# Kernel optimization log

Hardware: AMD Instinct MI355X
Metric: run time of the kernel (lower is better)

The kernel has to match this reference:

```python
import jax, jax.numpy as jnp
import numpy as np

# Grid derived from defaults: pc_range=(0,-40,-3,70.4,40,1), voxel=(0.2,0.2,4)
GX, GY = 352, 400          # round((70.4-0)/0.2), round((40-(-40))/0.2)
B, P = 4, 65536            # samples, points per sample
NSEG = B * GX * GY + 1     # dense pillar-id space + 1 sentinel for masked points
OUT_CH = 64
BN_EPS = 1e-3


def setup_inputs() -> dict:
    key = jax.random.key(0)
    k1, k2, k3 = jax.random.split(key, 3)
    xyz_min = jnp.array([0.0, -40.0, -3.0], jnp.float32)
    xyz_max = jnp.array([70.4, 40.0, 1.0], jnp.float32)
    xyz = jax.random.uniform(k1, (B, P, 3), jnp.float32, minval=xyz_min, maxval=xyz_max)
    rest = jax.random.normal(k2, (B, P, 4), jnp.float32)  # rcs, v_r, v_r_comp, time
    points = jnp.concatenate([xyz, rest], axis=-1)        # [B, P, 7]
    W = jax.random.normal(k3, (OUT_CH, 13), jnp.float32) * (1.0 / np.sqrt(13.0))
    gamma = jnp.ones((OUT_CH,), jnp.float32)
    beta = jnp.zeros((OUT_CH,), jnp.float32)
    return {"points": points, "W": W, "gamma": gamma, "beta": beta}


def reference(points, W, gamma, beta):
    Bn, Pn, _ = points.shape
    pts = points.reshape(Bn * Pn, 7)                      # [N, 7] (= torch points[:, 1:])
    dtype = pts.dtype
    voxel = jnp.array([0.2, 0.2, 4.0], dtype)
    pc_min = jnp.array([0.0, -40.0, -3.0], dtype)
    batch_idx = jnp.repeat(jnp.arange(Bn, dtype=jnp.int32), Pn)

    coords_f = (pts[:, :3] - pc_min) / voxel              # float voxel coords
    mask = ((coords_f[:, 0] >= 0) & (coords_f[:, 0] < GX)
            & (coords_f[:, 1] >= 0) & (coords_f[:, 1] < GY))
    coords = coords_f.astype(jnp.int32)                   # [N, 3] (cx, cy, cz)
    sentinel = Bn * GX * GY                               # trash segment for masked points
    lin = jnp.where(mask,
                    batch_idx * (GX * GY) + coords[:, 0] * GY + coords[:, 1],
                    sentinel)
    # torch.unique(..., return_inverse=True, dim=0) on (batch, cx, cy) rows ==
    # unique of the bijective linear id (same sorted order).
    unq, unq_inv = jnp.unique(lin, return_inverse=True, size=NSEG, fill_value=sentinel)

    cnt = jax.ops.segment_sum(jnp.ones((lin.shape[0], 1), dtype), unq_inv, num_segments=NSEG)
    mean_xyz = jax.ops.segment_sum(pts[:, :3], unq_inv, num_segments=NSEG) / jnp.maximum(cnt, 1.0)
    f_cluster = pts[:, :3] - mean_xyz[unq_inv]
    f_center = pts[:, :3] - (coords.astype(dtype) * voxel + voxel * 0.5 + pc_min)
    feats = jnp.concatenate([pts, f_cluster, f_center], axis=-1)   # [N, 13]

    # PFN layer (last_layer=True): Linear -> BN1d (training stats) -> ReLU
    x = feats @ W.T                                       # [N, 64]
    mu = x.mean(axis=0)
    var = x.var(axis=0)                                   # biased, as BN training
    x = jax.nn.relu((x - mu) * jax.lax.rsqrt(var + BN_EPS) * gamma + beta)

    fmax = jax.ops.segment_max(x, unq_inv, num_segments=NSEG)     # scatter_max
    x_max = fmax[unq_inv]                                 # gather back (PFN output)
    feat_max = jax.ops.segment_max(x_max, unq_inv, num_segments=NSEG)

    valid = (unq < sentinel)[:, None]                     # real pillars only
    feat_max = jnp.where(valid, feat_max, 0.0)            # padded/empty -> 0

    b = unq // (GX * GY)
    rem = unq % (GX * GY)
    cx = rem // GY
    cy = rem % GY
    coords_out = jnp.stack([b, cy, cx], axis=1).astype(jnp.int32)  # (batch, y, x)
    grid_size = jnp.array([GY, GX], jnp.int32)
    return feat_max, coords_out, grid_size
```

## Files before the change

kernel.cpp:

```cpp
#include <hip/hip_runtime.h>
#include <stdint.h>
#include <utility>

#define NPTS   262144
#define GXGY   140800
#define GYv    400
#define NSEG   563201
#define SENT   563200
#define NB_SCAN 275
#define PIL_BLOCKS 2048
#define MOM_BLOCKS 512

constexpr size_t alignup(size_t x) { return (x + 255) & ~(size_t)255; }
constexpr size_t O_CNT  = 0;
constexpr size_t O_SUMS = alignup(O_CNT + (size_t)NSEG * 4);
constexpr size_t O_MOM  = alignup(O_SUMS + (size_t)NSEG * 12);
constexpr size_t ZERO_BYTES = alignup(O_MOM + 104 * 4);
constexpr size_t O_PPTR = ZERO_BYTES;
constexpr size_t O_LINA = alignup(O_PPTR + (size_t)NSEG * 4);
constexpr size_t O_ROWI = alignup(O_LINA + (size_t)NPTS * 4);
constexpr size_t O_FEAT = alignup(O_ROWI + (size_t)NPTS * 16);
constexpr size_t O_BSO  = alignup(O_FEAT + (size_t)NPTS * 64);
constexpr size_t O_BSC  = alignup(O_BSO + NB_SCAN * 4);
constexpr size_t O_KP   = alignup(O_BSC + NB_SCAN * 4);
constexpr size_t O_WF   = alignup(O_KP + 256);
constexpr size_t O_SH   = alignup(O_WF + 832 * 4);

__device__ __forceinline__ int point_lin(float x, float y, int b, bool& mask) {
  float cxf = x / 0.2f;
  float cyf = (y + 40.0f) / 0.2f;
  int cx = (int)cxf, cy = (int)cyf;
  mask = (cxf >= 0.0f) && (cxf < 352.0f) && (cyf >= 0.0f) && (cyf < 400.0f);
  return mask ? (b * GXGY + cx * GYv + cy) : SENT;
}

__global__ __launch_bounds__(256) void k_count(const float* __restrict__ pts,
                                               unsigned int* __restrict__ cnt,
                                               float* __restrict__ sums,
                                               unsigned int* __restrict__ lina) {
  int i = blockIdx.x * 256 + threadIdx.x;
  if (i >= NPTS) return;
  const float* p = pts + (size_t)i * 7;
  float x = p[0], y = p[1], z = p[2];
  bool m;
  int lin = point_lin(x, y, i >> 16, m);
  lina[i] = (unsigned)lin;
  atomicAdd(&cnt[lin], 1u);
  atomicAdd(&sums[lin * 3 + 0], x);
  atomicAdd(&sums[lin * 3 + 1], y);
  atomicAdd(&sums[lin * 3 + 2], z);
}

__global__ __launch_bounds__(256) void k_scan1(const unsigned int* __restrict__ cnt,
                                               unsigned int* __restrict__ bso,
                                               unsigned int* __restrict__ bsc) {
  int t = threadIdx.x;
  int base = blockIdx.x * 2048 + t * 8;
  const uint4* c4 = (const uint4*)(cnt + base);
  uint4 a = c4[0], b = c4[1];
  unsigned so = (a.x > 0) + (a.y > 0) + (a.z > 0) + (a.w > 0) +
                (b.x > 0) + (b.y > 0) + (b.z > 0) + (b.w > 0);
  unsigned sc = a.x + a.y + a.z + a.w + b.x + b.y + b.z + b.w;
  for (int m = 1; m < 64; m <<= 1) { so += __shfl_xor(so, m); sc += __shfl_xor(sc, m); }
  __shared__ unsigned wo[4], wc[4];
  if ((t & 63) == 0) { wo[t >> 6] = so; wc[t >> 6] = sc; }
  __syncthreads();
  if (t == 0) {
    bso[blockIdx.x] = wo[0] + wo[1] + wo[2] + wo[3];
    bsc[blockIdx.x] = wc[0] + wc[1] + wc[2] + wc[3];
  }
}

__global__ __launch_bounds__(256) void k_scan3(const unsigned int* __restrict__ cnt,
                                               const unsigned int* __restrict__ bso,
                                               const unsigned int* __restrict__ bsc,
                                               uint4* __restrict__ rowinfo,
                                               unsigned int* __restrict__ pptr,
                                               unsigned int* __restrict__ kp) {
  int t = threadIdx.x;
  unsigned vo_m = 0, vc_m = 0, vo_a = 0;
  for (int e = t; e < NB_SCAN; e += 256) {
    unsigned o = bso[e], c = bsc[e];
    vo_a += o;
    if (e < (int)blockIdx.x) { vo_m += o; vc_m += c; }
  }
  for (int m = 1; m < 64; m <<= 1) {
    vo_m += __shfl_xor(vo_m, m);
    vc_m += __shfl_xor(vc_m, m);
    vo_a += __shfl_xor(vo_a, m);
  }
  __shared__ unsigned s0[4], s1[4], s2[4];
  int wv = t >> 6;
  if ((t & 63) == 0) { s0[wv] = vo_m; s1[wv] = vc_m; s2[wv] = vo_a; }
  __syncthreads();
  unsigned boo = s0[0] + s0[1] + s0[2] + s0[3];
  unsigned boc = s1[0] + s1[1] + s1[2] + s1[3];
  unsigned tot = s2[0] + s2[1] + s2[2] + s2[3];
  if (blockIdx.x == 0 && t == 0) *kp = tot;

  int base = blockIdx.x * 2048 + t * 8;
  const uint4* q = (const uint4*)(cnt + base);
  uint4 a = q[0], b = q[1];
  unsigned c[8] = {a.x, a.y, a.z, a.w, b.x, b.y, b.z, b.w};
  unsigned po[8], pc[8];
  unsigned so = 0, sc = 0;
#pragma unroll
  for (int k = 0; k < 8; k++) {
    po[k] = so; pc[k] = sc;
    so += (c[k] > 0); sc += c[k];
  }
  __shared__ unsigned sdo[256], sdc[256];
  __syncthreads();
  sdo[t] = so; sdc[t] = sc;
  __syncthreads();
  for (int off = 1; off < 256; off <<= 1) {
    unsigned ao = (t >= off) ? sdo[t - off] : 0u;
    unsigned ac = (t >= off) ? sdc[t - off] : 0u;
    __syncthreads();
    sdo[t] += ao; sdc[t] += ac;
    __syncthreads();
  }
  unsigned eo = sdo[t] - so + boo;
  unsigned ec = sdc[t] - sc + boc;
#pragma unroll
  for (int k = 0; k < 8; k++) {
    if (c[k] > 0) {
      unsigned r = eo + po[k];
      unsigned start = ec + pc[k];
      rowinfo[r] = make_uint4((unsigned)(base + k), start, c[k], 0u);
      pptr[base + k] = start;
    }
  }
}

__global__ __launch_bounds__(256) void k_sortfeat(const float* __restrict__ pts,
                                                  const unsigned int* __restrict__ lina,
                                                  const unsigned int* __restrict__ cnt,
                                                  const float* __restrict__ sums,
                                                  unsigned int* __restrict__ pptr,
                                                  float* __restrict__ feat) {
  int i = blockIdx.x * 256 + threadIdx.x;
  if (i >= NPTS) return;
  unsigned lin = lina[i];
  if (lin == SENT) return;
  const float* p = pts + (size_t)i * 7;
  float x = p[0], y = p[1], z = p[2];
  unsigned pos = atomicAdd(&pptr[lin], 1u);
  float cm = fmaxf((float)cnt[lin], 1.0f);
  float m0 = sums[lin * 3 + 0] / cm;
  float m1 = sums[lin * 3 + 1] / cm;
  float m2 = sums[lin * 3 + 2] / cm;
  int cx = (int)(x / 0.2f);
  int cy = (int)((y + 40.0f) / 0.2f);
  int cz = (int)((z + 3.0f) / 4.0f);
  float4 A = make_float4(x, y, z, p[3]);
  float4 B = make_float4(p[4], p[5], p[6], x - m0);
  float4 C = make_float4(y - m1, z - m2,
                         x - ((float)cx * 0.2f + 0.1f + 0.0f),
                         y - ((float)cy * 0.2f + 0.1f - 40.0f));
  float4 D = make_float4(z - ((float)cz * 4.0f + 2.0f - 3.0f), 0.f, 0.f, 0.f);
  float4* fb = (float4*)(feat + (size_t)pos * 16);
  fb[0] = A; fb[1] = B; fb[2] = C; fb[3] = D;
}

constexpr int tri_j(int t) { int j = 0; while (t >= 13 - j) { t -= 13 - j; j++; } return j; }
constexpr int tri_k(int t) { int j = 0; while (t >= 13 - j) { t -= 13 - j; j++; } return j + t; }

template<int G, size_t U>
__device__ __forceinline__ void accum_one(const float (&f)[13], float (&acc)[52]) {
  constexpr int E = G * 52 + (int)U;
  if constexpr (E < 13) {
    acc[U] += f[E];
  } else {
    constexpr int J = tri_j(E - 13);
    constexpr int K = tri_k(E - 13);
    acc[U] += f[J] * f[K];
  }
}
template<int G, size_t... Us>
__device__ __forceinline__ void accum_all(const float (&f)[13], float (&acc)[52],
                                          std::index_sequence<Us...>) {
  (accum_one<G, Us>(f, acc), ...);
}

template<int G>
__device__ __forceinline__ void moments_body(const float* __restrict__ feat,
                                             float* __restrict__ mom, int chunk) {
  float acc[52];
#pragma unroll
  for (int u = 0; u < 52; u++) acc[u] = 0.f;
#pragma unroll
  for (int r = 0; r < 4; r++) {
    int i = chunk * 1024 + r * 256 + threadIdx.x;
    const float4* fp = (const float4*)(feat + (size_t)i * 16);
    float4 A = fp[0], B = fp[1], C = fp[2], D = fp[3];
    float f[13] = {A.x, A.y, A.z, A.w, B.x, B.y, B.z, B.w, C.x, C.y, C.z, C.w, D.x};
    accum_all<G>(f, acc, std::make_index_sequence<52>{});
  }
  __shared__ float red[4][52];
  int wv = threadIdx.x >> 6, lane = threadIdx.x & 63;
#pragma unroll
  for (int u = 0; u < 52; u++) {
    float v = acc[u];
    v += __shfl_xor(v, 1);  v += __shfl_xor(v, 2);  v += __shfl_xor(v, 4);
    v += __shfl_xor(v, 8);  v += __shfl_xor(v, 16); v += __shfl_xor(v, 32);
    if (lane == 0) red[wv][u] = v;
  }
  __syncthreads();
  if (threadIdx.x < 52) {
    int u = threadIdx.x;
    atomicAdd(&mom[G * 52 + u], red[0][u] + red[1][u] + red[2][u] + red[3][u]);
  }
}

__global__ __launch_bounds__(256, 2) void k_moments(const float* __restrict__ feat,
                                                    float* __restrict__ mom) {
  int chunk = blockIdx.x >> 1;
  if ((blockIdx.x & 1) == 0) moments_body<0>(feat, mom, chunk);
  else                       moments_body<1>(feat, mom, chunk);
}

__global__ void k_bnfinal(const float* __restrict__ W,
                          const float* __restrict__ g,
                          const float* __restrict__ bta,
                          const float* __restrict__ mom,
                          float* __restrict__ wf,
                          float* __restrict__ sh) {
  int c = threadIdx.x;
  float w[13];
#pragma unroll
  for (int j = 0; j < 13; j++) w[j] = W[c * 13 + j];
  const float invN = 1.0f / (float)NPTS;
  float mu = 0.f;
#pragma unroll
  for (int j = 0; j < 13; j++) mu += w[j] * (mom[j] * invN);
  float e2 = 0.f;
  int mi = 13;
#pragma unroll
  for (int j = 0; j < 13; j++) {
#pragma unroll
    for (int k = j; k < 13; k++) {
      float coef = (j == k) ? 1.0f : 2.0f;
      e2 += coef * w[j] * w[k] * mom[mi];
      mi++;
    }
  }
  e2 *= invN;
  float var = e2 - mu * mu;
  float rsig = 1.0f / sqrtf(var + 1e-3f);
  float sc = g[c] * rsig;
#pragma unroll
  for (int j = 0; j < 13; j++) wf[c * 13 + j] = w[j] * sc;
  sh[c] = bta[c] - mu * sc;
}

__global__ __launch_bounds__(256) void k_pillar(const float* __restrict__ wf,
                                                const float* __restrict__ sh,
                                                const uint4* __restrict__ rowinfo,
                                                const unsigned int* __restrict__ kp_p,
                                                const float* __restrict__ feat,
                                                float* __restrict__ out) {
  int tid = threadIdx.x;
  int lane = tid & 15;
  int ch0 = lane * 4;
  float wr[52];
  float shv[4];
#pragma unroll
  for (int c4 = 0; c4 < 4; c4++) {
    shv[c4] = sh[ch0 + c4];
#pragma unroll
    for (int j = 0; j < 13; j++) wr[c4 * 13 + j] = wf[(ch0 + c4) * 13 + j];
  }
  unsigned kp = *kp_p;

  const int NGRP = PIL_BLOCKS * 16;
  for (int r = blockIdx.x * 16 + (tid >> 4); r < NSEG; r += NGRP) {
    float m0 = -3.4e38f, m1 = -3.4e38f, m2 = -3.4e38f, m3 = -3.4e38f;
    int b = 4, cy = 0, cx = 0;
    if ((unsigned)r < kp) {
      uint4 ri = rowinfo[r];
      unsigned id = ri.x, start = ri.y, n = ri.z;
      b = id / GXGY;
      unsigned rem = id - (unsigned)b * GXGY;
      cx = rem / GYv;
      cy = rem - cx * GYv;
      const float4* fb = (const float4*)(feat + (size_t)start * 16);
      for (unsigned p = 0; p < n; p++) {
        float4 A = fb[0], B = fb[1], C = fb[2], D = fb[3];
        fb += 4;
        float d0, d1, d2, d3;
#define DOT(dst, c4)                                                          \
        dst = shv[c4];                                                        \
        dst += wr[c4 * 13 + 0]  * A.x;  dst += wr[c4 * 13 + 1]  * A.y;        \
        dst += wr[c4 * 13 + 2]  * A.z;  dst += wr[c4 * 13 + 3]  * A.w;        \
        dst += wr[c4 * 13 + 4]  * B.x;  dst += wr[c4 * 13 + 5]  * B.y;        \
        dst += wr[c4 * 13 + 6]  * B.z;  dst += wr[c4 * 13 + 7]  * B.w;        \
        dst += wr[c4 * 13 + 8]  * C.x;  dst += wr[c4 * 13 + 9]  * C.y;        \
        dst += wr[c4 * 13 + 10] * C.z;  dst += wr[c4 * 13 + 11] * C.w;        \
        dst += wr[c4 * 13 + 12] * D.x;
        DOT(d0, 0) DOT(d1, 1) DOT(d2, 2) DOT(d3, 3)
#undef DOT
        m0 = fmaxf(m0, d0); m1 = fmaxf(m1, d1);
        m2 = fmaxf(m2, d2); m3 = fmaxf(m3, d3);
      }
    }
    float4 v = make_float4(fmaxf(m0, 0.f), fmaxf(m1, 0.f),
                           fmaxf(m2, 0.f), fmaxf(m3, 0.f));
    *(float4*)(out + (size_t)r * 64 + lane * 4) = v;
    if (lane == 0) {
      float* cc = out + (size_t)NSEG * 64 + (size_t)r * 3;
      cc[0] = (float)b;
      cc[1] = (float)cy;
      cc[2] = (float)cx;
    }
  }
  if (blockIdx.x == 0 && tid == 0) {
    float* g = out + (size_t)NSEG * 67;
    g[0] = 400.0f;
    g[1] = 352.0f;
  }
}

extern "C" void kernel_launch(void* const* d_in, const int* in_sizes, int n_in,
                              void* d_out, int out_size, void* d_ws, size_t ws_size,
                              hipStream_t stream) {
  const float* pts = (const float*)d_in[0];
  const float* W   = (const float*)d_in[1];
  const float* g   = (const float*)d_in[2];
  const float* bta = (const float*)d_in[3];
  float* out = (float*)d_out;
  char* ws = (char*)d_ws;

  unsigned int* cnt  = (unsigned int*)(ws + O_CNT);
  float*        sums = (float*)(ws + O_SUMS);
  float*        mom  = (float*)(ws + O_MOM);
  unsigned int* pptr = (unsigned int*)(ws + O_PPTR);
  unsigned int* lina = (unsigned int*)(ws + O_LINA);
  uint4*        rowi = (uint4*)(ws + O_ROWI);
  float*        feat = (float*)(ws + O_FEAT);
  unsigned int* bso  = (unsigned int*)(ws + O_BSO);
  unsigned int* bsc  = (unsigned int*)(ws + O_BSC);
  unsigned int* kp   = (unsigned int*)(ws + O_KP);
  float*        wf   = (float*)(ws + O_WF);
  float*        sh   = (float*)(ws + O_SH);
  (void)in_sizes; (void)n_in; (void)out_size; (void)ws_size;

  hipMemsetAsync(ws, 0, ZERO_BYTES, stream);

  k_count   <<<NPTS / 256, 256, 0, stream>>>(pts, cnt, sums, lina);
  k_scan1   <<<NB_SCAN, 256, 0, stream>>>(cnt, bso, bsc);
  k_scan3   <<<NB_SCAN, 256, 0, stream>>>(cnt, bso, bsc, rowi, pptr, kp);
  k_sortfeat<<<NPTS / 256, 256, 0, stream>>>(pts, lina, cnt, sums, pptr, feat);
  k_moments <<<MOM_BLOCKS, 256, 0, stream>>>(feat, mom);
  k_bnfinal <<<1, 64, 0, stream>>>(W, g, bta, mom, wf, sh);
  k_pillar  <<<PIL_BLOCKS, 256, 0, stream>>>(wf, sh, rowi, kp, feat, out);
}
```

Baseline: 287.9 us.

## Fuse moments into sort-feature kernel and fold BN finalize into pillar kernel

Feature-moment accumulation now happens while features are built in the scatter kernel, so the separate pass that re-reads the whole feature buffer goes away. The batch-norm finalize kernel is removed: every pillar block recomputes scale and shift from the moments and raw weights in shared memory, then applies scale and shift after the dot product. Two launches are removed, but 1024 blocks now issue atomics to the moments buffer, every pillar block redoes the finalize, and each point's max step gains an extra multiply-add. Masked points now also contribute to the moments, matching the earlier behaviour where sentinel slots were counted.

```diff
diff --git a/kernel.cpp b/kernel.cpp
--- a/kernel.cpp
+++ b/kernel.cpp
@@ -9,7 +9,6 @@
 #define SENT   563200
 #define NB_SCAN 275
 #define PIL_BLOCKS 2048
-#define MOM_BLOCKS 512
 
 constexpr size_t alignup(size_t x) { return (x + 255) & ~(size_t)255; }
 constexpr size_t O_CNT  = 0;
@@ -23,8 +22,6 @@
 constexpr size_t O_BSO  = alignup(O_FEAT + (size_t)NPTS * 64);
 constexpr size_t O_BSC  = alignup(O_BSO + NB_SCAN * 4);
 constexpr size_t O_KP   = alignup(O_BSC + NB_SCAN * 4);
-constexpr size_t O_WF   = alignup(O_KP + 256);
-constexpr size_t O_SH   = alignup(O_WF + 832 * 4);
 
 __device__ __forceinline__ int point_lin(float x, float y, int b, bool& mask) {
   float cxf = x / 0.2f;
@@ -133,19 +130,56 @@
   }
 }
 
-__global__ __launch_bounds__(256) void k_sortfeat(const float* __restrict__ pts,
-                                                  const unsigned int* __restrict__ lina,
-                                                  const unsigned int* __restrict__ cnt,
-                                                  const float* __restrict__ sums,
-                                                  unsigned int* __restrict__ pptr,
-                                                  float* __restrict__ feat) {
+constexpr int tri_j(int t) { int j = 0; while (t >= 13 - j) { t -= 13 - j; j++; } return j; }
+constexpr int tri_k(int t) { int j = 0; while (t >= 13 - j) { t -= 13 - j; j++; } return j + t; }
+
+template<int G, size_t U>
+__device__ __forceinline__ void accum_one(const float (&f)[13], float (&acc)[52]) {
+  constexpr int E = G * 52 + (int)U;
+  if constexpr (E < 13) {
+    acc[U] = f[E];
+  } else {
+    constexpr int J = tri_j(E - 13);
+    constexpr int K = tri_k(E - 13);
+    acc[U] = f[J] * f[K];
+  }
+}
+template<int G, size_t... Us>
+__device__ __forceinline__ void accum_all(const float (&f)[13], float (&acc)[52],
+                                          std::index_sequence<Us...>) {
+  (accum_one<G, Us>(f, acc), ...);
+}
+
+__device__ __forceinline__ void block_reduce_acc(float (&acc)[52],
+                                                 float* __restrict__ mom, int base) {
+  __shared__ float red[4][52];
+  int wv = threadIdx.x >> 6, lane = threadIdx.x & 63;
+#pragma unroll
+  for (int u = 0; u < 52; u++) {
+    float v = acc[u];
+    v += __shfl_xor(v, 1);  v += __shfl_xor(v, 2);  v += __shfl_xor(v, 4);
+    v += __shfl_xor(v, 8);  v += __shfl_xor(v, 16); v += __shfl_xor(v, 32);
+    if (lane == 0) red[wv][u] = v;
+  }
+  __syncthreads();
+  if (threadIdx.x < 52) {
+    int u = threadIdx.x;
+    atomicAdd(&mom[base + u], red[0][u] + red[1][u] + red[2][u] + red[3][u]);
+  }
+  __syncthreads();
+}
+
+__global__ __launch_bounds__(256, 2) void k_sfm(const float* __restrict__ pts,
+                                                const unsigned int* __restrict__ lina,
+                                                const unsigned int* __restrict__ cnt,
+                                                const float* __restrict__ sums,
+                                                unsigned int* __restrict__ pptr,
+                                                float* __restrict__ feat,
+                                                float* __restrict__ mom) {
   int i = blockIdx.x * 256 + threadIdx.x;
-  if (i >= NPTS) return;
   unsigned lin = lina[i];
-  if (lin == SENT) return;
   const float* p = pts + (size_t)i * 7;
   float x = p[0], y = p[1], z = p[2];
-  unsigned pos = atomicAdd(&pptr[lin], 1u);
   float cm = fmaxf((float)cnt[lin], 1.0f);
   float m0 = sums[lin * 3 + 0] / cm;
   float m1 = sums[lin * 3 + 1] / cm;
@@ -153,123 +187,73 @@
   int cx = (int)(x / 0.2f);
   int cy = (int)((y + 40.0f) / 0.2f);
   int cz = (int)((z + 3.0f) / 4.0f);
-  float4 A = make_float4(x, y, z, p[3]);
-  float4 B = make_float4(p[4], p[5], p[6], x - m0);
-  float4 C = make_float4(y - m1, z - m2,
-                         x - ((float)cx * 0.2f + 0.1f + 0.0f),
-                         y - ((float)cy * 0.2f + 0.1f - 40.0f));
-  float4 D = make_float4(z - ((float)cz * 4.0f + 2.0f - 3.0f), 0.f, 0.f, 0.f);
-  float4* fb = (float4*)(feat + (size_t)pos * 16);
-  fb[0] = A; fb[1] = B; fb[2] = C; fb[3] = D;
-}
-
-constexpr int tri_j(int t) { int j = 0; while (t >= 13 - j) { t -= 13 - j; j++; } return j; }
-constexpr int tri_k(int t) { int j = 0; while (t >= 13 - j) { t -= 13 - j; j++; } return j + t; }
-
-template<int G, size_t U>
-__device__ __forceinline__ void accum_one(const float (&f)[13], float (&acc)[52]) {
-  constexpr int E = G * 52 + (int)U;
-  if constexpr (E < 13) {
-    acc[U] += f[E];
-  } else {
-    constexpr int J = tri_j(E - 13);
-    constexpr int K = tri_k(E - 13);
-    acc[U] += f[J] * f[K];
-  }
-}
-template<int G, size_t... Us>
-__device__ __forceinline__ void accum_all(const float (&f)[13], float (&acc)[52],
-                                          std::index_sequence<Us...>) {
-  (accum_one<G, Us>(f, acc), ...);
-}
-
-template<int G>
-__device__ __forceinline__ void moments_body(const float* __restrict__ feat,
-                                             float* __restrict__ mom, int chunk) {
+  float f[13] = {x, y, z, p[3], p[4], p[5], p[6],
+                 x - m0, y - m1, z - m2,
+                 x - ((float)cx * 0.2f + 0.1f + 0.0f),
+                 y - ((float)cy * 0.2f + 0.1f - 40.0f),
+                 z - ((float)cz * 4.0f + 2.0f - 3.0f)};
+  if (lin != SENT) {
+    unsigned pos = atomicAdd(&pptr[lin], 1u);
+    float4* fb = (float4*)(feat + (size_t)pos * 16);
+    fb[0] = make_float4(f[0], f[1], f[2], f[3]);
+    fb[1] = make_float4(f[4], f[5], f[6], f[7]);
+    fb[2] = make_float4(f[8], f[9], f[10], f[11]);
+    fb[3] = make_float4(f[12], 0.f, 0.f, 0.f);
+  }
   float acc[52];
-#pragma unroll
-  for (int u = 0; u < 52; u++) acc[u] = 0.f;
-#pragma unroll
-  for (int r = 0; r < 4; r++) {
-    int i = chunk * 1024 + r * 256 + threadIdx.x;
-    const float4* fp = (const float4*)(feat + (size_t)i * 16);
-    float4 A = fp[0], B = fp[1], C = fp[2], D = fp[3];
-    float f[13] = {A.x, A.y, A.z, A.w, B.x, B.y, B.z, B.w, C.x, C.y, C.z, C.w, D.x};
-    accum_all<G>(f, acc, std::make_index_sequence<52>{});
-  }
-  __shared__ float red[4][52];
-  int wv = threadIdx.x >> 6, lane = threadIdx.x & 63;
-#pragma unroll
-  for (int u = 0; u < 52; u++) {
-    float v = acc[u];
-    v += __shfl_xor(v, 1);  v += __shfl_xor(v, 2);  v += __shfl_xor(v, 4);
-    v += __shfl_xor(v, 8);  v += __shfl_xor(v, 16); v += __shfl_xor(v, 32);
-    if (lane == 0) red[wv][u] = v;
-  }
-  __syncthreads();
-  if (threadIdx.x < 52) {
-    int u = threadIdx.x;
-    atomicAdd(&mom[G * 52 + u], red[0][u] + red[1][u] + red[2][u] + red[3][u]);
-  }
-}
-
-__global__ __launch_bounds__(256, 2) void k_moments(const float* __restrict__ feat,
-                                                    float* __restrict__ mom) {
-  int chunk = blockIdx.x >> 1;
-  if ((blockIdx.x & 1) == 0) moments_body<0>(feat, mom, chunk);
-  else                       moments_body<1>(feat, mom, chunk);
-}
-
-__global__ void k_bnfinal(const float* __restrict__ W,
-                          const float* __restrict__ g,
-                          const float* __restrict__ bta,
-                          const float* __restrict__ mom,
-                          float* __restrict__ wf,
-                          float* __restrict__ sh) {
-  int c = threadIdx.x;
-  float w[13];
-#pragma unroll
-  for (int j = 0; j < 13; j++) w[j] = W[c * 13 + j];
-  const float invN = 1.0f / (float)NPTS;
-  float mu = 0.f;
-#pragma unroll
-  for (int j = 0; j < 13; j++) mu += w[j] * (mom[j] * invN);
-  float e2 = 0.f;
-  int mi = 13;
-#pragma unroll
-  for (int j = 0; j < 13; j++) {
-#pragma unroll
-    for (int k = j; k < 13; k++) {
-      float coef = (j == k) ? 1.0f : 2.0f;
-      e2 += coef * w[j] * w[k] * mom[mi];
-      mi++;
-    }
-  }
-  e2 *= invN;
-  float var = e2 - mu * mu;
-  float rsig = 1.0f / sqrtf(var + 1e-3f);
-  float sc = g[c] * rsig;
-#pragma unroll
-  for (int j = 0; j < 13; j++) wf[c * 13 + j] = w[j] * sc;
-  sh[c] = bta[c] - mu * sc;
-}
-
-__global__ __launch_bounds__(256) void k_pillar(const float* __restrict__ wf,
-                                                const float* __restrict__ sh,
+  accum_all<0>(f, acc, std::make_index_sequence<52>{});
+  block_reduce_acc(acc, mom, 0);
+  accum_all<1>(f, acc, std::make_index_sequence<52>{});
+  block_reduce_acc(acc, mom, 52);
+}
+
+__global__ __launch_bounds__(256) void k_pillar(const float* __restrict__ W,
+                                                const float* __restrict__ g,
+                                                const float* __restrict__ bta,
+                                                const float* __restrict__ mom,
                                                 const uint4* __restrict__ rowinfo,
                                                 const unsigned int* __restrict__ kp_p,
                                                 const float* __restrict__ feat,
                                                 float* __restrict__ out) {
+  __shared__ float LW[832];
+  __shared__ float LS[128];
   int tid = threadIdx.x;
+  for (int t = tid; t < 832; t += 256) LW[t] = W[t];
+  __syncthreads();
+  if (tid < 64) {
+    const float invN = 1.0f / (float)NPTS;
+    float mu = 0.f;
+#pragma unroll
+    for (int j = 0; j < 13; j++) mu += LW[tid * 13 + j] * (mom[j] * invN);
+    float e2 = 0.f;
+    int mi = 13;
+#pragma unroll
+    for (int j = 0; j < 13; j++) {
+#pragma unroll
+      for (int k = j; k < 13; k++) {
+        float coef = (j == k) ? 1.0f : 2.0f;
+        e2 += coef * LW[tid * 13 + j] * LW[tid * 13 + k] * mom[mi];
+        mi++;
+      }
+    }
+    e2 *= invN;
+    float var = e2 - mu * mu;
+    float rsig = 1.0f / sqrtf(var + 1e-3f);
+    float sc = g[tid] * rsig;
+    LS[tid] = sc;
+    LS[64 + tid] = bta[tid] - mu * sc;
+  }
+  __syncthreads();
+
   int lane = tid & 15;
   int ch0 = lane * 4;
-  float wr[52];
-  float shv[4];
+  float wr[52], scv[4], shv[4];
 #pragma unroll
   for (int c4 = 0; c4 < 4; c4++) {
-    shv[c4] = sh[ch0 + c4];
-#pragma unroll
-    for (int j = 0; j < 13; j++) wr[c4 * 13 + j] = wf[(ch0 + c4) * 13 + j];
+    scv[c4] = LS[ch0 + c4];
+    shv[c4] = LS[64 + ch0 + c4];
+#pragma unroll
+    for (int j = 0; j < 13; j++) wr[c4 * 13 + j] = LW[(ch0 + c4) * 13 + j];
   }
   unsigned kp = *kp_p;
 
@@ -290,7 +274,7 @@
         fb += 4;
         float d0, d1, d2, d3;
 #define DOT(dst, c4)                                                          \
-        dst = shv[c4];                                                        \
+        dst = 0.f;                                                            \
         dst += wr[c4 * 13 + 0]  * A.x;  dst += wr[c4 * 13 + 1]  * A.y;        \
         dst += wr[c4 * 13 + 2]  * A.z;  dst += wr[c4 * 13 + 3]  * A.w;        \
         dst += wr[c4 * 13 + 4]  * B.x;  dst += wr[c4 * 13 + 5]  * B.y;        \
@@ -300,8 +284,10 @@
         dst += wr[c4 * 13 + 12] * D.x;
         DOT(d0, 0) DOT(d1, 1) DOT(d2, 2) DOT(d3, 3)
 #undef DOT
-        m0 = fmaxf(m0, d0); m1 = fmaxf(m1, d1);
-        m2 = fmaxf(m2, d2); m3 = fmaxf(m3, d3);
+        m0 = fmaxf(m0, d0 * scv[0] + shv[0]);
+        m1 = fmaxf(m1, d1 * scv[1] + shv[1]);
+        m2 = fmaxf(m2, d2 * scv[2] + shv[2]);
+        m3 = fmaxf(m3, d3 * scv[3] + shv[3]);
       }
     }
     float4 v = make_float4(fmaxf(m0, 0.f), fmaxf(m1, 0.f),
@@ -315,9 +301,9 @@
     }
   }
   if (blockIdx.x == 0 && tid == 0) {
-    float* g = out + (size_t)NSEG * 67;
-    g[0] = 400.0f;
-    g[1] = 352.0f;
+    float* gr = out + (size_t)NSEG * 67;
+    gr[0] = 400.0f;
+    gr[1] = 352.0f;
   }
 }
 
@@ -341,17 +327,13 @@
   unsigned int* bso  = (unsigned int*)(ws + O_BSO);
   unsigned int* bsc  = (unsigned int*)(ws + O_BSC);
   unsigned int* kp   = (unsigned int*)(ws + O_KP);
-  float*        wf   = (float*)(ws + O_WF);
-  float*        sh   = (float*)(ws + O_SH);
   (void)in_sizes; (void)n_in; (void)out_size; (void)ws_size;
 
   hipMemsetAsync(ws, 0, ZERO_BYTES, stream);
 
-  k_count   <<<NPTS / 256, 256, 0, stream>>>(pts, cnt, sums, lina);
-  k_scan1   <<<NB_SCAN, 256, 0, stream>>>(cnt, bso, bsc);
-  k_scan3   <<<NB_SCAN, 256, 0, stream>>>(cnt, bso, bsc, rowi, pptr, kp);
-  k_sortfeat<<<NPTS / 256, 256, 0, stream>>>(pts, lina, cnt, sums, pptr, feat);
-  k_moments <<<MOM_BLOCKS, 256, 0, stream>>>(feat, mom);
-  k_bnfinal <<<1, 64, 0, stream>>>(W, g, bta, mom, wf, sh);
-  k_pillar  <<<PIL_BLOCKS, 256, 0, stream>>>(wf, sh, rowi, kp, feat, out);
-}
+  k_count <<<NPTS / 256, 256, 0, stream>>>(pts, cnt, sums, lina);
+  k_scan1 <<<NB_SCAN, 256, 0, stream>>>(cnt, bso, bsc);
+  k_scan3 <<<NB_SCAN, 256, 0, stream>>>(cnt, bso, bsc, rowi, pptr, kp);
+  k_sfm   <<<NPTS / 256, 256, 0, stream>>>(pts, lina, cnt, sums, pptr, feat, mom);
+  k_pillar<<<PIL_BLOCKS, 256, 0, stream>>>(W, g, bta, mom, rowi, kp, feat, out);
+}
```

New measurement: 301.2 us. +4.6%, slower.
